# Performance work log

Hardware: AMD Instinct MI355X
Metric: run time of the kernel (lower is better)

Reference implementation:

```python
import jax, jax.numpy as jnp
import numpy as np

EPS = 1e-5
CONV_THRESHOLD = 0.0


def setup_inputs() -> dict:
    key = jax.random.key(0)
    ks = jax.random.split(key, 16)
    B, F = 65536, 256
    H1, H2 = 1024, 512
    d_in = F + 1  # raw features + 1 scalar conv feature
    inp = {
        "x": jax.random.normal(ks[0], (B, F), dtype=jnp.float32),
        # layer 1: Linear(d_in, H1) + BatchNorm1d(H1)
        "W1": jax.random.normal(ks[1], (d_in, H1), dtype=jnp.float32) * (1.0 / np.sqrt(d_in)),
        "b1": jax.random.normal(ks[2], (H1,), dtype=jnp.float32) * 0.01,
        "g1": jnp.ones((H1,), jnp.float32) + 0.1 * jax.random.normal(ks[3], (H1,), dtype=jnp.float32),
        "be1": jax.random.normal(ks[4], (H1,), dtype=jnp.float32) * 0.01,
        "m1": jax.random.normal(ks[5], (H1,), dtype=jnp.float32) * 0.1,
        "v1": jax.random.uniform(ks[6], (H1,), dtype=jnp.float32, minval=0.5, maxval=1.5),
        # layer 2: Linear(H1, H2) + BatchNorm1d(H2)
        "W2": jax.random.normal(ks[7], (H1, H2), dtype=jnp.float32) * (1.0 / np.sqrt(H1)),
        "b2": jax.random.normal(ks[8], (H2,), dtype=jnp.float32) * 0.01,
        "g2": jnp.ones((H2,), jnp.float32) + 0.1 * jax.random.normal(ks[9], (H2,), dtype=jnp.float32),
        "be2": jax.random.normal(ks[10], (H2,), dtype=jnp.float32) * 0.01,
        "m2": jax.random.normal(ks[11], (H2,), dtype=jnp.float32) * 0.1,
        "v2": jax.random.uniform(ks[12], (H2,), dtype=jnp.float32, minval=0.5, maxval=1.5),
        # output head: Linear(H2, 1)
        "W3": jax.random.normal(ks[13], (H2, 1), dtype=jnp.float32) * (1.0 / np.sqrt(H2)),
        "b3": jax.random.normal(ks[14], (1,), dtype=jnp.float32) * 0.01,
    }
    return inp


def _bn(h, g, be, m, v):
    # eval-mode BatchNorm1d with running statistics
    return g * (h - m) * jax.lax.rsqrt(v + EPS) + be


def reference(x, W1, b1, g1, be1, m1, v1, W2, b2, g2, be2, m2, v2, W3, b3):
    # Batched replacement of the per-sample numpy threshold conv:
    # the Conv filter reduces the whole sample patch with a mean and thresholds it,
    # producing one binary scalar feature per sample.  [B, 1]
    conv_feat = jnp.where(jnp.mean(x, axis=1, keepdims=True) > CONV_THRESHOLD, 1.0, 0.0).astype(x.dtype)
    h = jnp.concatenate([x, conv_feat], axis=1)  # [B, F+1]
    h = jax.nn.relu(_bn(h @ W1 + b1, g1, be1, m1, v1))  # [B, H1]
    h = jax.nn.relu(_bn(h @ W2 + b2, g2, be2, m2, v2))  # [B, H2]
    return jax.nn.sigmoid(h @ W3 + b3)  # [B, 1]
```

## Files before the change

kernel.cpp:

```cpp
#include <hip/hip_runtime.h>
#include <hip/hip_bf16.h>
#include <hip/hip_cooperative_groups.h>
#include <cstdint>
#include <cstddef>

namespace cg = cooperative_groups;

typedef __bf16 bf16_t;
typedef bf16_t bf16x8 __attribute__((ext_vector_type(8)));
typedef float f32x4 __attribute__((ext_vector_type(4)));

#define BN_EPS 1e-5f

__device__ __forceinline__ void async_load16(const bf16_t* g, bf16_t* lds) {
  __builtin_amdgcn_global_load_lds(
      (__attribute__((address_space(1))) uint32_t*)(g),
      (__attribute__((address_space(3))) uint32_t*)(lds),
      16, 0, 0);
}

__global__ void prep_weights_kernel(const float* __restrict__ W1, const float* __restrict__ W2,
                                    const float* b1, const float* g1, const float* be1,
                                    const float* m1, const float* v1,
                                    const float* b2, const float* g2, const float* be2,
                                    const float* m2, const float* v2,
                                    bf16_t* __restrict__ W1T, bf16_t* __restrict__ W2T,
                                    float* s1, float* t1, float* s2, float* t2,
                                    float* w1last) {
  const int b = blockIdx.x;
  if (b < 192) {
    const float* src;
    bf16_t* dst;
    int R, C, bx, by;
    if (b < 64) { src = W1; dst = W1T; R = 256; C = 1024; bx = b & 15; by = b >> 4; }
    else        { src = W2; dst = W2T; R = 1024; C = 512; bx = (b - 64) & 7; by = (b - 64) >> 3; }
    __shared__ bf16_t tile[64][66];
    const int r0 = by * 64, c0 = bx * 64;
    const int tc = threadIdx.x & 63;
    const int tr4 = threadIdx.x >> 6;
#pragma unroll
    for (int i = 0; i < 16; ++i) {
      int r = i * 4 + tr4;
      tile[r][tc] = (bf16_t)src[(size_t)(r0 + r) * C + c0 + tc];
    }
    __syncthreads();
#pragma unroll
    for (int i = 0; i < 16; ++i) {
      int rr = i * 4 + tr4;
      dst[(size_t)(c0 + rr) * R + r0 + tc] = tile[tc][rr];
    }
  } else {
    for (int i = threadIdx.x; i < 1024; i += 256) {
      float s = g1[i] * rsqrtf(v1[i] + BN_EPS);
      s1[i] = s;
      t1[i] = be1[i] - m1[i] * s + b1[i] * s;
      w1last[i] = W1[256 * 1024 + i];
      if (i < 512) {
        float s2v = g2[i] * rsqrtf(v2[i] + BN_EPS);
        s2[i] = s2v;
        t2[i] = be2[i] - m2[i] * s2v + b2[i] * s2v;
      }
    }
  }
}

__device__ __forceinline__ void gemm1_body(
    const float* __restrict__ x, const bf16_t* __restrict__ W1T,
    const float* __restrict__ s1, const float* __restrict__ t1,
    const float* __restrict__ w1last, bf16_t* __restrict__ h1,
    unsigned char* smem, int mTile, int lane, int w) {
  bf16_t* As = (bf16_t*)smem;
  bf16_t* Bs = (bf16_t*)(smem + 65536);
  float* convs = (float*)(smem + 65536);
  const int l15 = lane & 15;
  const int quad = lane >> 4;

  {
    const int rsub = lane >> 5;
    const int c = lane & 31;
#pragma unroll
    for (int i = 0; i < 16; ++i) {
      int row = w * 32 + i * 2 + rsub;
      const float* gx = x + (size_t)(mTile + row) * 256 + c * 8;
      const float4 a = *(const float4*)gx;
      const float4 bq = *(const float4*)(gx + 4);
      float s = a.x + a.y + a.z + a.w + bq.x + bq.y + bq.z + bq.w;
      bf16x8 v = {(bf16_t)a.x, (bf16_t)a.y, (bf16_t)a.z, (bf16_t)a.w,
                  (bf16_t)bq.x, (bf16_t)bq.y, (bf16_t)bq.z, (bf16_t)bq.w};
      *(bf16x8*)(As + row * 256 + (c ^ (row & 7)) * 8) = v;
#pragma unroll
      for (int m = 1; m <= 16; m <<= 1) s += __shfl_xor(s, m);
      if (c == 0) convs[row] = (s > 0.0f) ? 1.0f : 0.0f;
    }
  }
  __syncthreads();

  unsigned cmask = 0;
#pragma unroll
  for (int ti = 0; ti < 8; ++ti)
#pragma unroll
    for (int r = 0; r < 4; ++r)
      if (convs[ti * 16 + quad * 4 + r] > 0.5f) cmask |= (1u << (ti * 4 + r));
  __syncthreads();

  bf16_t* BsW = Bs + w * 2048;
  const int srow = lane >> 2;
  const int schunk = (lane & 3) ^ ((lane >> 3) & 3);
  const int rchunk = quad ^ ((l15 >> 1) & 3);

  for (int j = 0; j < 4; ++j) {
    const int colbase = j * 256 + w * 64;
    f32x4 acc[8][4];
#pragma unroll
    for (int i = 0; i < 8; ++i)
#pragma unroll
      for (int t = 0; t < 4; ++t) {
        f32x4 z = {0.f, 0.f, 0.f, 0.f};
        acc[i][t] = z;
      }

    const bf16_t* gB = W1T + (size_t)(colbase + srow) * 256 + schunk * 8;

    for (int ks = 0; ks < 8; ++ks) {
#pragma unroll
      for (int i = 0; i < 4; ++i)
        async_load16(gB + (size_t)(i * 16) * 256 + ks * 32, BsW + i * 512 + lane * 8);
      asm volatile("s_waitcnt vmcnt(0)" ::: "memory");

      bf16x8 af[8], bfr[4];
#pragma unroll
      for (int tj = 0; tj < 4; ++tj)
        bfr[tj] = *(const bf16x8*)(BsW + (tj * 16 + l15) * 32 + rchunk * 8);
#pragma unroll
      for (int ti = 0; ti < 8; ++ti)
        af[ti] = *(const bf16x8*)(As + (ti * 16 + l15) * 256 + ((ks * 4 + quad) ^ (l15 & 7)) * 8);
#pragma unroll
      for (int ti = 0; ti < 8; ++ti)
#pragma unroll
        for (int tj = 0; tj < 4; ++tj)
          acc[ti][tj] = __builtin_amdgcn_mfma_f32_16x16x32_bf16(af[ti], bfr[tj], acc[ti][tj], 0, 0, 0);
    }

    float sc[4], tcv[4], wl[4];
#pragma unroll
    for (int tj = 0; tj < 4; ++tj) {
      int c = colbase + tj * 16 + l15;
      sc[tj] = s1[c];
      tcv[tj] = t1[c];
      wl[tj] = w1last[c];
    }
#pragma unroll
    for (int ti = 0; ti < 8; ++ti)
#pragma unroll
      for (int r = 0; r < 4; ++r) {
        int row = mTile + ti * 16 + quad * 4 + r;
        size_t base = (size_t)row * 1024 + colbase;
        const float cfv = ((cmask >> (ti * 4 + r)) & 1u) ? 1.0f : 0.0f;
#pragma unroll
        for (int tj = 0; tj < 4; ++tj) {
          float z = acc[ti][tj][r] + cfv * wl[tj];
          z = fmaxf(z * sc[tj] + tcv[tj], 0.f);
          h1[base + tj * 16 + l15] = (bf16_t)z;
        }
      }
  }
}

__device__ __forceinline__ void gemm2_task_body(
    const bf16_t* __restrict__ h1, const bf16_t* __restrict__ W2T,
    const float* __restrict__ s2, const float* __restrict__ t2,
    const float* __restrict__ W3, float* __restrict__ partials,
    unsigned char* smem, int task, int lane, int w) {
  bf16_t* As2 = (bf16_t*)smem;
  bf16_t* Bs2 = (bf16_t*)(smem + 32768);
  const int l15 = lane & 15;
  const int quad = lane >> 4;
  const int sRow = lane >> 2;
  const int sColSwz = ((lane & 3) ^ ((lane >> 3) & 3)) * 8;
  const int rchunk8 = (quad ^ ((l15 >> 1) & 3)) * 8;

  const int mt = (task >> 5) * 8 + (task & 7);
  const int mTile2 = mt * 256;
  const int nt = (task >> 3) & 3;
  const int nTile = nt * 128;

  const bf16_t* gA = h1 + (size_t)(mTile2 + w * 64 + sRow) * 1024 + sColSwz;
  const bf16_t* gB = W2T + (size_t)(nTile + w * 32 + sRow) * 1024 + sColSwz;
  bf16_t* lA0 = As2 + (w * 64) * 32;
  bf16_t* lB0 = Bs2 + (w * 32) * 32;

  f32x4 acc[4][8];
#pragma unroll
  for (int i = 0; i < 4; ++i)
#pragma unroll
    for (int j = 0; j < 8; ++j) {
      f32x4 z = {0.f, 0.f, 0.f, 0.f};
      acc[i][j] = z;
    }

  __syncthreads();

#define STAGE2(buf, k0)                                                     \
  do {                                                                      \
    bf16_t* lA = lA0 + (buf)*8192;                                          \
    bf16_t* lB = lB0 + (buf)*4096;                                          \
    async_load16(gA + (k0), lA);                                            \
    async_load16(gA + (size_t)16 * 1024 + (k0), lA + 16 * 32);              \
    async_load16(gA + (size_t)32 * 1024 + (k0), lA + 32 * 32);              \
    async_load16(gA + (size_t)48 * 1024 + (k0), lA + 48 * 32);              \
    async_load16(gB + (k0), lB);                                            \
    async_load16(gB + (size_t)16 * 1024 + (k0), lB + 16 * 32);              \
  } while (0)

  STAGE2(0, 0);
  __syncthreads();

  int buf = 0;
  for (int k0 = 0; k0 < 1024; k0 += 32) {
    if (k0 + 32 < 1024) STAGE2(buf ^ 1, k0 + 32);

    bf16x8 af[4], bfr[8];
#pragma unroll
    for (int t = 0; t < 4; ++t)
      af[t] = *(const bf16x8*)(As2 + buf * 8192 + (w * 64 + t * 16 + l15) * 32 + rchunk8);
#pragma unroll
    for (int t = 0; t < 8; ++t)
      bfr[t] = *(const bf16x8*)(Bs2 + buf * 4096 + (t * 16 + l15) * 32 + rchunk8);
#pragma unroll
    for (int ti = 0; ti < 4; ++ti)
#pragma unroll
      for (int tj = 0; tj < 8; ++tj)
        acc[ti][tj] = __builtin_amdgcn_mfma_f32_16x16x32_bf16(af[ti], bfr[tj], acc[ti][tj], 0, 0, 0);

    if (k0 + 32 < 1024) {
      __syncthreads();
      buf ^= 1;
    }
  }
#undef STAGE2

  float sc[8], tc[8], w3c[8];
#pragma unroll
  for (int tj = 0; tj < 8; ++tj) {
    int c = nTile + tj * 16 + l15;
    sc[tj] = s2[c];
    tc[tj] = t2[c];
    w3c[tj] = W3[c];
  }
#pragma unroll
  for (int ti = 0; ti < 4; ++ti)
#pragma unroll
    for (int r = 0; r < 4; ++r) {
      float pv = 0.f;
#pragma unroll
      for (int tj = 0; tj < 8; ++tj) {
        float z = fmaxf(acc[ti][tj][r] * sc[tj] + tc[tj], 0.f);
        pv += z * w3c[tj];
      }
#pragma unroll
      for (int m = 1; m <= 8; m <<= 1) pv += __shfl_xor(pv, m);
      if (l15 == 0)
        partials[(size_t)nt * 65536 + mTile2 + w * 64 + ti * 16 + quad * 4 + r] = pv;
    }
}

__global__ __launch_bounds__(256, 2) void gemm1_kernel(
    const float* __restrict__ x, const bf16_t* __restrict__ W1T,
    const float* __restrict__ s1, const float* __restrict__ t1,
    const float* __restrict__ w1last, bf16_t* __restrict__ h1) {
  __shared__ __align__(16) unsigned char smem[81920];
  gemm1_body(x, W1T, s1, t1, w1last, h1, smem, blockIdx.x * 128,
             threadIdx.x & 63, threadIdx.x >> 6);
}

__global__ __launch_bounds__(256, 2) void gemm2_kernel(
    const bf16_t* __restrict__ h1, const bf16_t* __restrict__ W2T,
    const float* __restrict__ s2, const float* __restrict__ t2,
    const float* __restrict__ W3, float* __restrict__ partials) {
  __shared__ __align__(16) unsigned char smem[49152];
  gemm2_task_body(h1, W2T, s2, t2, W3, partials, smem, blockIdx.x,
                  threadIdx.x & 63, threadIdx.x >> 6);
}

__global__ void sigmoid_partials_kernel(const float* __restrict__ partials,
                                        const float* __restrict__ b3,
                                        float* __restrict__ out) {
  int i = blockIdx.x * 256 + threadIdx.x;
  float z = partials[i] + partials[65536 + i] + partials[2 * 65536 + i] +
            partials[3 * 65536 + i] + b3[0];
  out[i] = 1.0f / (1.0f + expf(-z));
}

__global__ __launch_bounds__(256, 2) void fused_mlp_coop(
    const float* __restrict__ x,
    const bf16_t* __restrict__ W1T, const bf16_t* __restrict__ W2T,
    const float* __restrict__ s1, const float* __restrict__ t1,
    const float* __restrict__ w1last,
    const float* __restrict__ s2, const float* __restrict__ t2,
    const float* __restrict__ W3, const float* __restrict__ b3,
    bf16_t* __restrict__ h1, float* __restrict__ partials,
    float* __restrict__ out) {
  __shared__ __align__(16) unsigned char smem[81920];
  cg::grid_group grid = cg::this_grid();
  const int tid = threadIdx.x;
  const int lane = tid & 63;
  const int w = tid >> 6;

  gemm1_body(x, W1T, s1, t1, w1last, h1, smem, blockIdx.x * 128, lane, w);

  grid.sync();

  gemm2_task_body(h1, W2T, s2, t2, W3, partials, smem, blockIdx.x, lane, w);
  gemm2_task_body(h1, W2T, s2, t2, W3, partials, smem, blockIdx.x + 512, lane, w);

  grid.sync();

  if (tid < 128) {
    int r = blockIdx.x * 128 + tid;
    float z = partials[r] + partials[65536 + r] + partials[2 * 65536 + r] +
              partials[3 * 65536 + r] + b3[0];
    out[r] = 1.0f / (1.0f + expf(-z));
  }
}

extern "C" void kernel_launch(void* const* d_in, const int* in_sizes, int n_in,
                              void* d_out, int out_size, void* d_ws, size_t ws_size,
                              hipStream_t stream) {
  const float* x = (const float*)d_in[0];
  const float* W1 = (const float*)d_in[1];
  const float* b1 = (const float*)d_in[2];
  const float* g1 = (const float*)d_in[3];
  const float* be1 = (const float*)d_in[4];
  const float* m1 = (const float*)d_in[5];
  const float* v1 = (const float*)d_in[6];
  const float* W2 = (const float*)d_in[7];
  const float* b2 = (const float*)d_in[8];
  const float* g2 = (const float*)d_in[9];
  const float* be2 = (const float*)d_in[10];
  const float* m2 = (const float*)d_in[11];
  const float* v2 = (const float*)d_in[12];
  const float* W3 = (const float*)d_in[13];
  const float* b3 = (const float*)d_in[14];
  float* out = (float*)d_out;

  char* p = (char*)d_ws;
  bf16_t* h1 = (bf16_t*)p;       p += (size_t)65536 * 1024 * 2;
  float* partials = (float*)p;   p += (size_t)4 * 65536 * 4;
  bf16_t* W1T = (bf16_t*)p;      p += (size_t)1024 * 256 * 2;
  bf16_t* W2T = (bf16_t*)p;      p += (size_t)512 * 1024 * 2;
  float* w1last = (float*)p;     p += 1024 * 4;
  float* s1 = (float*)p;         p += 1024 * 4;
  float* t1 = (float*)p;         p += 1024 * 4;
  float* s2 = (float*)p;         p += 512 * 4;
  float* t2 = (float*)p;         p += 512 * 4;

  prep_weights_kernel<<<193, 256, 0, stream>>>(W1, W2, b1, g1, be1, m1, v1,
                                               b2, g2, be2, m2, v2,
                                               W1T, W2T, s1, t1, s2, t2, w1last);

  int dev = 0;
  (void)hipGetDevice(&dev);
  int coopOk = 0;
  (void)hipDeviceGetAttribute(&coopOk, hipDeviceAttributeCooperativeLaunch, dev);
  int numCU = 0;
  (void)hipDeviceGetAttribute(&numCU, hipDeviceAttributeMultiprocessorCount, dev);
  int maxBlk = 0;
  (void)hipOccupancyMaxActiveBlocksPerMultiprocessor(&maxBlk, fused_mlp_coop, 256, 0);

  bool useCoop = (coopOk != 0) && ((long)maxBlk * (long)numCU >= 512L);
  if (useCoop) {
    void* args[] = {(void*)&x, (void*)&W1T, (void*)&W2T, (void*)&s1, (void*)&t1,
                    (void*)&w1last, (void*)&s2, (void*)&t2, (void*)&W3, (void*)&b3,
                    (void*)&h1, (void*)&partials, (void*)&out};
    hipError_t e = hipLaunchCooperativeKernel((const void*)fused_mlp_coop,
                                              dim3(512), dim3(256), args, 0, stream);
    if (e != hipSuccess) useCoop = false;
  }
  if (!useCoop) {
    gemm1_kernel<<<512, 256, 0, stream>>>(x, W1T, s1, t1, w1last, h1);
    gemm2_kernel<<<1024, 256, 0, stream>>>(h1, W2T, s2, t2, W3, partials);
    sigmoid_partials_kernel<<<256, 256, 0, stream>>>(partials, b3, out);
  }
}
```

Baseline: 251.4 us.

## Prefetch W1 tiles during MFMA and triple-buffer GEMM2 LDS pipeline

In GEMM1, the next k-step's W1 tile is now issued as an async global-to-LDS load right after the current fragments are read into registers, so it overlaps the MFMA work instead of stalling before it. GEMM2 moves from double to triple buffering with rotating LDS offsets, uses explicit vmcnt waits and raw s_barrier in place of __syncthreads, and sets a higher wave priority around the MFMA blocks. GEMM2's LDS use grows from 48KB to 72KB, which may limit how many blocks fit per CU. The hand-counted vmcnt values have to match the number of in-flight loads exactly.

```diff
diff --git a/kernel.cpp b/kernel.cpp
--- a/kernel.cpp
+++ b/kernel.cpp
@@ -121,10 +121,11 @@
 
     const bf16_t* gB = W1T + (size_t)(colbase + srow) * 256 + schunk * 8;
 
+#pragma unroll
+    for (int i = 0; i < 4; ++i)
+      async_load16(gB + (size_t)(i * 16) * 256, BsW + i * 512 + lane * 8);
+
     for (int ks = 0; ks < 8; ++ks) {
-#pragma unroll
-      for (int i = 0; i < 4; ++i)
-        async_load16(gB + (size_t)(i * 16) * 256 + ks * 32, BsW + i * 512 + lane * 8);
       asm volatile("s_waitcnt vmcnt(0)" ::: "memory");
 
       bf16x8 af[8], bfr[4];
@@ -134,11 +135,21 @@
 #pragma unroll
       for (int ti = 0; ti < 8; ++ti)
         af[ti] = *(const bf16x8*)(As + (ti * 16 + l15) * 256 + ((ks * 4 + quad) ^ (l15 & 7)) * 8);
+
+      asm volatile("s_waitcnt lgkmcnt(0)" ::: "memory");
+      if (ks < 7) {
+#pragma unroll
+        for (int i = 0; i < 4; ++i)
+          async_load16(gB + (size_t)(i * 16) * 256 + (ks + 1) * 32, BsW + i * 512 + lane * 8);
+      }
+
+      __builtin_amdgcn_s_setprio(1);
 #pragma unroll
       for (int ti = 0; ti < 8; ++ti)
 #pragma unroll
         for (int tj = 0; tj < 4; ++tj)
           acc[ti][tj] = __builtin_amdgcn_mfma_f32_16x16x32_bf16(af[ti], bfr[tj], acc[ti][tj], 0, 0, 0);
+      __builtin_amdgcn_s_setprio(0);
     }
 
     float sc[4], tcv[4], wl[4];
@@ -172,7 +183,7 @@
     const float* __restrict__ W3, float* __restrict__ partials,
     unsigned char* smem, int task, int lane, int w) {
   bf16_t* As2 = (bf16_t*)smem;
-  bf16_t* Bs2 = (bf16_t*)(smem + 32768);
+  bf16_t* Bs2 = (bf16_t*)(smem + 49152);
   const int l15 = lane & 15;
   const int quad = lane >> 4;
   const int sRow = lane >> 2;
@@ -200,10 +211,10 @@
 
   __syncthreads();
 
-#define STAGE2(buf, k0)                                                     \
+#define STAGE2(aoff, boff, k0)                                              \
   do {                                                                      \
-    bf16_t* lA = lA0 + (buf)*8192;                                          \
-    bf16_t* lB = lB0 + (buf)*4096;                                          \
+    bf16_t* lA = lA0 + (aoff);                                              \
+    bf16_t* lB = lB0 + (boff);                                              \
     async_load16(gA + (k0), lA);                                            \
     async_load16(gA + (size_t)16 * 1024 + (k0), lA + 16 * 32);              \
     async_load16(gA + (size_t)32 * 1024 + (k0), lA + 32 * 32);              \
@@ -212,39 +223,52 @@
     async_load16(gB + (size_t)16 * 1024 + (k0), lB + 16 * 32);              \
   } while (0)
 
-  STAGE2(0, 0);
-  __syncthreads();
-
-  int buf = 0;
-  for (int k0 = 0; k0 < 1024; k0 += 32) {
-    if (k0 + 32 < 1024) STAGE2(buf ^ 1, k0 + 32);
+  STAGE2(0, 0, 0);
+  STAGE2(8192, 4096, 32);
+
+  int aCur = 0, aN1 = 8192, aN2 = 16384;
+  int bCur = 0, bN1 = 4096, bN2 = 8192;
+
+  for (int t = 0; t < 32; ++t) {
+    if (t < 30) {
+      STAGE2(aN2, bN2, (t + 2) * 32);
+      asm volatile("s_waitcnt vmcnt(12)" ::: "memory");
+    } else if (t == 30) {
+      asm volatile("s_waitcnt vmcnt(6)" ::: "memory");
+    } else {
+      asm volatile("s_waitcnt vmcnt(0)" ::: "memory");
+    }
+    asm volatile("s_barrier" ::: "memory");
 
     bf16x8 af[4], bfr[8];
 #pragma unroll
-    for (int t = 0; t < 4; ++t)
-      af[t] = *(const bf16x8*)(As2 + buf * 8192 + (w * 64 + t * 16 + l15) * 32 + rchunk8);
-#pragma unroll
-    for (int t = 0; t < 8; ++t)
-      bfr[t] = *(const bf16x8*)(Bs2 + buf * 4096 + (t * 16 + l15) * 32 + rchunk8);
+    for (int ti = 0; ti < 4; ++ti)
+      af[ti] = *(const bf16x8*)(As2 + aCur + (w * 64 + ti * 16 + l15) * 32 + rchunk8);
+#pragma unroll
+    for (int tj = 0; tj < 8; ++tj)
+      bfr[tj] = *(const bf16x8*)(Bs2 + bCur + (tj * 16 + l15) * 32 + rchunk8);
+
+    __builtin_amdgcn_s_setprio(1);
 #pragma unroll
     for (int ti = 0; ti < 4; ++ti)
 #pragma unroll
       for (int tj = 0; tj < 8; ++tj)
         acc[ti][tj] = __builtin_amdgcn_mfma_f32_16x16x32_bf16(af[ti], bfr[tj], acc[ti][tj], 0, 0, 0);
-
-    if (k0 + 32 < 1024) {
-      __syncthreads();
-      buf ^= 1;
-    }
+    __builtin_amdgcn_s_setprio(0);
+
+    asm volatile("s_barrier" ::: "memory");
+
+    int tmp = aCur; aCur = aN1; aN1 = aN2; aN2 = tmp;
+    tmp = bCur; bCur = bN1; bN1 = bN2; bN2 = tmp;
   }
 #undef STAGE2
 
-  float sc[8], tc[8], w3c[8];
+  float sc[8], tcs[8], w3c[8];
 #pragma unroll
   for (int tj = 0; tj < 8; ++tj) {
     int c = nTile + tj * 16 + l15;
     sc[tj] = s2[c];
-    tc[tj] = t2[c];
+    tcs[tj] = t2[c];
     w3c[tj] = W3[c];
   }
 #pragma unroll
@@ -254,7 +278,7 @@
       float pv = 0.f;
 #pragma unroll
       for (int tj = 0; tj < 8; ++tj) {
-        float z = fmaxf(acc[ti][tj][r] * sc[tj] + tc[tj], 0.f);
+        float z = fmaxf(acc[ti][tj][r] * sc[tj] + tcs[tj], 0.f);
         pv += z * w3c[tj];
       }
 #pragma unroll
@@ -277,7 +301,7 @@
     const bf16_t* __restrict__ h1, const bf16_t* __restrict__ W2T,
     const float* __restrict__ s2, const float* __restrict__ t2,
     const float* __restrict__ W3, float* __restrict__ partials) {
-  __shared__ __align__(16) unsigned char smem[49152];
+  __shared__ __align__(16) unsigned char smem[73728];
   gemm2_task_body(h1, W2T, s2, t2, W3, partials, smem, blockIdx.x,
                   threadIdx.x & 63, threadIdx.x >> 6);
 }
```

Result: slower. 262.6 us (+4.4%).
